# Optimization experiments

Hardware: AMD Instinct MI355X
Metric: run time of the kernel (lower is better)

The kernel has to match this reference:

```python
import jax, jax.numpy as jnp
import numpy as np

ALPHA = 1.0

def setup_inputs() -> dict:
    key = jax.random.key(0)
    k1, k2 = jax.random.split(key)
    x = jax.random.normal(k1, (65536, 512), dtype=jnp.float32)
    clusters = jax.random.normal(k2, (256, 512), dtype=jnp.float32)
    return {"x": x, "clusters": clusters}

def reference(x, clusters):
    # Squared Euclidean distance to each centroid via the GEMM expansion
    x2 = jnp.sum(x * x, axis=1, keepdims=True)            # (B, 1)
    c2 = jnp.sum(clusters * clusters, axis=1)             # (K,)
    cross = x @ clusters.T                                # (B, K) GEMM
    d2 = jnp.maximum(x2 + c2 - 2.0 * cross, 0.0)          # (B, K)
    # Student-t kernel (DEC soft assignment)
    q = 1.0 / (1.0 + d2 / ALPHA)
    q = q ** ((ALPHA + 1.0) / 2.0)
    q = q / jnp.sum(q, axis=1, keepdims=True)             # row-normalize
    return q
```

## Files before the change

kernel.cpp:

```cpp
#include <hip/hip_runtime.h>
#include <hip/hip_bf16.h>


typedef __attribute__((ext_vector_type(8))) short short8v;
typedef __attribute__((ext_vector_type(4))) float f32x4;

#define DDIM 512
#define KCL  256
#define BM   64
#define NT   256
#define NTILES 16
#define BTILE  8192

__device__ __forceinline__ short f2bf(float f) {
    __hip_bfloat16 h = __float2bfloat16(f);
    return __builtin_bit_cast(short, h);
}

__device__ __forceinline__ void glds16(const void* g, void* l) {
    __builtin_amdgcn_global_load_lds(
        (const __attribute__((address_space(1))) unsigned int*)g,
        (__attribute__((address_space(3))) unsigned int*)l, 16, 0, 0);
}

__global__ void prep(const float* __restrict__ cl, short* __restrict__ wsB,
                     float* __restrict__ wsC2) {
    const int t = threadIdx.x;
    if (blockIdx.x < 64) {
        const int u = blockIdx.x * 256 + t;
        const int img = u >> 10, gi = u & 1023;
        const int g = gi >> 6, lq = (gi >> 4) & 3, l15 = gi & 15;
        const float* src = cl + (size_t)(g * 16 + l15) * DDIM + img * 32 + lq * 8;
        float4 a = *(const float4*)src;
        float4 b = *(const float4*)(src + 4);
        short8v s;
        s[0]=f2bf(a.x); s[1]=f2bf(a.y); s[2]=f2bf(a.z); s[3]=f2bf(a.w);
        s[4]=f2bf(b.x); s[5]=f2bf(b.y); s[6]=f2bf(b.z); s[7]=f2bf(b.w);
        *(short8v*)&wsB[(size_t)u * 8] = s;
    } else {
        const int cidx = (blockIdx.x - 64) * 16 + (t >> 4);
        const int j = t & 15;
        const float* src = cl + (size_t)cidx * DDIM + j * 32;
        float s = 0.f;
#pragma unroll
        for (int i = 0; i < 8; ++i) {
            float4 v = ((const float4*)src)[i];
            s += v.x*v.x + v.y*v.y + v.z*v.z + v.w*v.w;
        }
        s += __shfl_xor(s, 1); s += __shfl_xor(s, 2);
        s += __shfl_xor(s, 4); s += __shfl_xor(s, 8);
        if (j == 0) wsC2[cidx] = s;
    }
}

#define SFENCE() __builtin_amdgcn_sched_barrier(0)
#define BARV0()  asm volatile("s_waitcnt vmcnt(0) lgkmcnt(0)\ns_barrier" ::: "memory")

__global__ __launch_bounds__(NT, 3)
void dec_main(const float* __restrict__ x, const short* __restrict__ wsB,
              const float* __restrict__ wsC2, float* __restrict__ out) {
    __shared__ __align__(16) short lBd[2][BTILE];
    __shared__ __align__(16) float lAf[2][2048];
    __shared__ float s_x2[BM];
    __shared__ float s_rs[4][BM];

    const int t = threadIdx.x, lane = t & 63, w = t >> 6;
    const int cg = w;
    const int l15 = lane & 15, lq = lane >> 4;
    const int row0 = blockIdx.x * BM;

    const int rA = ((t >> 7) << 4) + (t & 15);
    const int cA = (((t >> 4) & 3) << 3) + (((t >> 6) & 1) << 2);
    const float* ga0 = x + (size_t)(row0 + rA) * DDIM + cA;
    const float* ga1 = x + (size_t)(row0 + rA + 32) * DDIM + cA;

    f32x4 acc[4][4];
#pragma unroll
    for (int m = 0; m < 4; ++m)
#pragma unroll
        for (int n = 0; n < 4; ++n) acc[m][n] = (f32x4){0.f,0.f,0.f,0.f};
    float x2p[4] = {0.f, 0.f, 0.f, 0.f};

#define GLDSA(TT, P)                                                 \
    {  glds16(ga0 + (TT) * 32, &lAf[P][t * 4]);                      \
       glds16(ga1 + (TT) * 32, &lAf[P][t * 4 + 1024]); }

#define GLDSB(TT, P)                                                 \
    {  const short* s_ = wsB + (size_t)(TT) * BTILE;                 \
       short* d_ = &lBd[P][0];                                       \
       glds16(s_ + t * 8,        d_ + t * 8);                        \
       glds16(s_ + 2048 + t * 8, d_ + 2048 + t * 8);                 \
       glds16(s_ + 4096 + t * 8, d_ + 4096 + t * 8);                 \
       glds16(s_ + 6144 + t * 8, d_ + 6144 + t * 8); }

#define MSTEP(P)                                                                 \
    {  short8v b0 = *(const short8v*)&lBd[P][(cg*4+0)*512 + lane*8];             \
       short8v b1 = *(const short8v*)&lBd[P][(cg*4+1)*512 + lane*8];             \
       short8v b2 = *(const short8v*)&lBd[P][(cg*4+2)*512 + lane*8];             \
       short8v b3 = *(const short8v*)&lBd[P][(cg*4+3)*512 + lane*8];             \
       _Pragma("unroll")                                                         \
       for (int m = 0; m < 4; ++m) {                                             \
           float4 alo = *(const float4*)&lAf[P][m*512 + lane*4];                 \
           float4 ahi = *(const float4*)&lAf[P][m*512 + 256 + lane*4];           \
           short8v af;                                                           \
           af[0]=f2bf(alo.x); af[1]=f2bf(alo.y); af[2]=f2bf(alo.z); af[3]=f2bf(alo.w); \
           af[4]=f2bf(ahi.x); af[5]=f2bf(ahi.y); af[6]=f2bf(ahi.z); af[7]=f2bf(ahi.w); \
           if (w == 0)                                                           \
               x2p[m] += alo.x*alo.x + alo.y*alo.y + alo.z*alo.z + alo.w*alo.w   \
                       + ahi.x*ahi.x + ahi.y*ahi.y + ahi.z*ahi.z + ahi.w*ahi.w;  \
           acc[m][0] = __builtin_amdgcn_mfma_f32_16x16x32_bf16(af, b0, acc[m][0], 0,0,0); \
           acc[m][1] = __builtin_amdgcn_mfma_f32_16x16x32_bf16(af, b1, acc[m][1], 0,0,0); \
           acc[m][2] = __builtin_amdgcn_mfma_f32_16x16x32_bf16(af, b2, acc[m][2], 0,0,0); \
           acc[m][3] = __builtin_amdgcn_mfma_f32_16x16x32_bf16(af, b3, acc[m][3], 0,0,0); \
       } }

#define ITER(J)                                                                  \
    {  if ((J) + 1 < NTILES) { GLDSA((J)+1, ((J)+1)&1); GLDSB((J)+1, ((J)+1)&1); } \
       SFENCE();                                                                 \
       MSTEP((J)&1);                                                             \
       if ((J) + 1 < NTILES) { BARV0(); }                                        \
       SFENCE(); }

    GLDSA(0, 0); GLDSB(0, 0);
    BARV0();
    SFENCE();

    ITER( 0) ITER( 1) ITER( 2) ITER( 3)
    ITER( 4) ITER( 5) ITER( 6) ITER( 7)
    ITER( 8) ITER( 9) ITER(10) ITER(11)
    ITER(12) ITER(13) ITER(14) ITER(15)

#pragma unroll
    for (int m = 0; m < 4; ++m) {
        float v = x2p[m];
        v += __shfl_xor(v, 16); v += __shfl_xor(v, 32);
        if (w == 0 && lq == 0) s_x2[m*16 + l15] = v;
    }
    __syncthreads();

    float c2a[4];
#pragma unroll
    for (int n = 0; n < 4; ++n) c2a[n] = wsC2[cg*64 + n*16 + l15];

#pragma unroll
    for (int m = 0; m < 4; ++m)
#pragma unroll
        for (int n = 0; n < 4; ++n)
#pragma unroll
            for (int r = 0; r < 4; ++r) {
                const int rw = m*16 + lq*4 + r;
                float d2 = fmaxf(s_x2[rw] + c2a[n] - 2.0f * acc[m][n][r], 0.0f);
                acc[m][n][r] = 1.0f / (1.0f + d2);
            }

#pragma unroll
    for (int m = 0; m < 4; ++m)
#pragma unroll
        for (int r = 0; r < 4; ++r) {
            float p = acc[m][0][r] + acc[m][1][r] + acc[m][2][r] + acc[m][3][r];
            p += __shfl_xor(p, 1); p += __shfl_xor(p, 2);
            p += __shfl_xor(p, 4); p += __shfl_xor(p, 8);
            if (l15 == 0) s_rs[cg][m*16 + lq*4 + r] = p;
        }
    __syncthreads();

#pragma unroll
    for (int m = 0; m < 4; ++m)
#pragma unroll
        for (int r = 0; r < 4; ++r) {
            const int rw = m*16 + lq*4 + r;
            const float rinv = 1.0f / (s_rs[0][rw] + s_rs[1][rw] + s_rs[2][rw] + s_rs[3][rw]);
            float* o = out + (size_t)(row0 + rw) * KCL + cg*64 + l15;
#pragma unroll
            for (int n = 0; n < 4; ++n)
                o[n * 16] = acc[m][n][r] * rinv;
        }
}

extern "C" void kernel_launch(void* const* d_in, const int* in_sizes, int n_in,
                              void* d_out, int out_size, void* d_ws, size_t ws_size,
                              hipStream_t stream) {
    const float* x  = (const float*)d_in[0];
    const float* cl = (const float*)d_in[1];
    float* out = (float*)d_out;
    short* wsB  = (short*)d_ws;
    float* wsC2 = (float*)((char*)d_ws + (size_t)NTILES * BTILE * sizeof(short));

    prep<<<80, 256, 0, stream>>>(cl, wsB, wsC2);
    const int B = in_sizes[0] / DDIM;
    dec_main<<<B / BM, NT, 0, stream>>>(x, wsB, wsC2, out);
}
```

Before: 60.26 us.

## Double block tile to 128 rows and prefetch A two stages ahead

Doubles the rows per block to 128 with 512 threads (8 waves, split into 2 row groups x 4 column groups), so each staged centroid tile is reused across twice as many rows and B-loading per thread halves. The x tile now uses a triple-buffered LDS ring loaded two iterations ahead, and barriers wait with vmcnt(2) so the next A load can stay in flight across the barrier. Scratch arrays for row norms and row sums reuse the A buffer, with an extra barrier added before reuse. LDS per block grows to about 80KB and the grid halves, which may reduce occupancy and the number of blocks available per CU.

```diff
diff --git a/kernel.cpp b/kernel.cpp
--- a/kernel.cpp
+++ b/kernel.cpp
@@ -7,8 +7,8 @@
 
 #define DDIM 512
 #define KCL  256
-#define BM   64
-#define NT   256
+#define BM   128
+#define NT   512
 #define NTILES 16
 #define BTILE  8192
 
@@ -54,25 +54,26 @@
 }
 
 #define SFENCE() __builtin_amdgcn_sched_barrier(0)
+#define BARV2()  asm volatile("s_waitcnt vmcnt(2) lgkmcnt(0)\ns_barrier" ::: "memory")
 #define BARV0()  asm volatile("s_waitcnt vmcnt(0) lgkmcnt(0)\ns_barrier" ::: "memory")
 
-__global__ __launch_bounds__(NT, 3)
+__global__ __launch_bounds__(NT, 4)
 void dec_main(const float* __restrict__ x, const short* __restrict__ wsB,
               const float* __restrict__ wsC2, float* __restrict__ out) {
+    __shared__ __align__(16) float lAf[3][4096];
     __shared__ __align__(16) short lBd[2][BTILE];
-    __shared__ __align__(16) float lAf[2][2048];
-    __shared__ float s_x2[BM];
-    __shared__ float s_rs[4][BM];
+    float* const s_x2 = &lAf[0][0];
+    float* const s_rs = &lAf[0][0] + BM;
 
     const int t = threadIdx.x, lane = t & 63, w = t >> 6;
-    const int cg = w;
+    const int rg = w >> 2, cg = w & 3;
     const int l15 = lane & 15, lq = lane >> 4;
     const int row0 = blockIdx.x * BM;
 
     const int rA = ((t >> 7) << 4) + (t & 15);
     const int cA = (((t >> 4) & 3) << 3) + (((t >> 6) & 1) << 2);
     const float* ga0 = x + (size_t)(row0 + rA) * DDIM + cA;
-    const float* ga1 = x + (size_t)(row0 + rA + 32) * DDIM + cA;
+    const float* ga1 = x + (size_t)(row0 + rA + 64) * DDIM + cA;
 
     f32x4 acc[4][4];
 #pragma unroll
@@ -83,29 +84,26 @@
 
 #define GLDSA(TT, P)                                                 \
     {  glds16(ga0 + (TT) * 32, &lAf[P][t * 4]);                      \
-       glds16(ga1 + (TT) * 32, &lAf[P][t * 4 + 1024]); }
+       glds16(ga1 + (TT) * 32, &lAf[P][t * 4 + 2048]); }
 
 #define GLDSB(TT, P)                                                 \
     {  const short* s_ = wsB + (size_t)(TT) * BTILE;                 \
-       short* d_ = &lBd[P][0];                                       \
-       glds16(s_ + t * 8,        d_ + t * 8);                        \
-       glds16(s_ + 2048 + t * 8, d_ + 2048 + t * 8);                 \
-       glds16(s_ + 4096 + t * 8, d_ + 4096 + t * 8);                 \
-       glds16(s_ + 6144 + t * 8, d_ + 6144 + t * 8); }
-
-#define MSTEP(P)                                                                 \
-    {  short8v b0 = *(const short8v*)&lBd[P][(cg*4+0)*512 + lane*8];             \
-       short8v b1 = *(const short8v*)&lBd[P][(cg*4+1)*512 + lane*8];             \
-       short8v b2 = *(const short8v*)&lBd[P][(cg*4+2)*512 + lane*8];             \
-       short8v b3 = *(const short8v*)&lBd[P][(cg*4+3)*512 + lane*8];             \
+       glds16(s_ + t * 8,        &lBd[P][t * 8]);                    \
+       glds16(s_ + 4096 + t * 8, &lBd[P][4096 + t * 8]); }
+
+#define MSTEP(AP, BP)                                                            \
+    {  short8v b0 = *(const short8v*)&lBd[BP][(cg*4+0)*512 + lane*8];            \
+       short8v b1 = *(const short8v*)&lBd[BP][(cg*4+1)*512 + lane*8];            \
+       short8v b2 = *(const short8v*)&lBd[BP][(cg*4+2)*512 + lane*8];            \
+       short8v b3 = *(const short8v*)&lBd[BP][(cg*4+3)*512 + lane*8];            \
        _Pragma("unroll")                                                         \
        for (int m = 0; m < 4; ++m) {                                             \
-           float4 alo = *(const float4*)&lAf[P][m*512 + lane*4];                 \
-           float4 ahi = *(const float4*)&lAf[P][m*512 + 256 + lane*4];           \
+           float4 alo = *(const float4*)&lAf[AP][(rg*4+m)*512 + lane*4];         \
+           float4 ahi = *(const float4*)&lAf[AP][(rg*4+m)*512 + 256 + lane*4];   \
            short8v af;                                                           \
            af[0]=f2bf(alo.x); af[1]=f2bf(alo.y); af[2]=f2bf(alo.z); af[3]=f2bf(alo.w); \
            af[4]=f2bf(ahi.x); af[5]=f2bf(ahi.y); af[6]=f2bf(ahi.z); af[7]=f2bf(ahi.w); \
-           if (w == 0)                                                           \
+           if (cg == 0)                                                          \
                x2p[m] += alo.x*alo.x + alo.y*alo.y + alo.z*alo.z + alo.w*alo.w   \
                        + ahi.x*ahi.x + ahi.y*ahi.y + ahi.z*ahi.z + ahi.w*ahi.w;  \
            acc[m][0] = __builtin_amdgcn_mfma_f32_16x16x32_bf16(af, b0, acc[m][0], 0,0,0); \
@@ -114,27 +112,46 @@
            acc[m][3] = __builtin_amdgcn_mfma_f32_16x16x32_bf16(af, b3, acc[m][3], 0,0,0); \
        } }
 
-#define ITER(J)                                                                  \
-    {  if ((J) + 1 < NTILES) { GLDSA((J)+1, ((J)+1)&1); GLDSB((J)+1, ((J)+1)&1); } \
+#define ITER(J, AC, AN, BC, BN)                                                  \
+    {  if ((J) + 1 < NTILES) { GLDSB((J)+1, BN); }                               \
+       if ((J) + 2 < NTILES) { GLDSA((J)+2, AN); }                               \
        SFENCE();                                                                 \
-       MSTEP((J)&1);                                                             \
-       if ((J) + 1 < NTILES) { BARV0(); }                                        \
+       MSTEP(AC, BC);                                                            \
+       SFENCE();                                                                 \
+       if ((J) + 2 < NTILES) { BARV2(); }                                        \
+       else if ((J) + 1 < NTILES) { BARV0(); }                                   \
        SFENCE(); }
 
-    GLDSA(0, 0); GLDSB(0, 0);
-    BARV0();
+    GLDSA(0, 0);
+    GLDSB(0, 0);
+    GLDSA(1, 1);
     SFENCE();
-
-    ITER( 0) ITER( 1) ITER( 2) ITER( 3)
-    ITER( 4) ITER( 5) ITER( 6) ITER( 7)
-    ITER( 8) ITER( 9) ITER(10) ITER(11)
-    ITER(12) ITER(13) ITER(14) ITER(15)
-
+    BARV2();
+    SFENCE();
+
+    ITER( 0, 0, 2, 0, 1)
+    ITER( 1, 1, 0, 1, 0)
+    ITER( 2, 2, 1, 0, 1)
+    ITER( 3, 0, 2, 1, 0)
+    ITER( 4, 1, 0, 0, 1)
+    ITER( 5, 2, 1, 1, 0)
+    ITER( 6, 0, 2, 0, 1)
+    ITER( 7, 1, 0, 1, 0)
+    ITER( 8, 2, 1, 0, 1)
+    ITER( 9, 0, 2, 1, 0)
+    ITER(10, 1, 0, 0, 1)
+    ITER(11, 2, 1, 1, 0)
+    ITER(12, 0, 2, 0, 1)
+    ITER(13, 1, 0, 1, 0)
+    ITER(14, 2, 1, 0, 1)
+    ITER(15, 0, 0, 1, 1)
+
+    __syncthreads();
 #pragma unroll
     for (int m = 0; m < 4; ++m) {
         float v = x2p[m];
         v += __shfl_xor(v, 16); v += __shfl_xor(v, 32);
-        if (w == 0 && lq == 0) s_x2[m*16 + l15] = v;
+        if (cg == 0 && lq == 0) s_x2[rg*64 + m*16 + l15] = v;
     }
     __syncthreads();
 
@@ -148,7 +165,7 @@
         for (int n = 0; n < 4; ++n)
 #pragma unroll
             for (int r = 0; r < 4; ++r) {
-                const int rw = m*16 + lq*4 + r;
+                const int rw = rg*64 + m*16 + lq*4 + r;
                 float d2 = fmaxf(s_x2[rw] + c2a[n] - 2.0f * acc[m][n][r], 0.0f);
                 acc[m][n][r] = 1.0f / (1.0f + d2);
             }
@@ -160,7 +177,7 @@
             float p = acc[m][0][r] + acc[m][1][r] + acc[m][2][r] + acc[m][3][r];
             p += __shfl_xor(p, 1); p += __shfl_xor(p, 2);
             p += __shfl_xor(p, 4); p += __shfl_xor(p, 8);
-            if (l15 == 0) s_rs[cg][m*16 + lq*4 + r] = p;
+            if (l15 == 0) s_rs[cg*BM + rg*64 + m*16 + lq*4 + r] = p;
         }
     __syncthreads();
 
@@ -168,8 +185,9 @@
     for (int m = 0; m < 4; ++m)
 #pragma unroll
         for (int r = 0; r < 4; ++r) {
-            const int rw = m*16 + lq*4 + r;
-            const float rinv = 1.0f / (s_rs[0][rw] + s_rs[1][rw] + s_rs[2][rw] + s_rs[3][rw]);
+            const int rw = rg*64 + m*16 + lq*4 + r;
+            const float rinv = 1.0f / (s_rs[rw] + s_rs[BM + rw]
+                                     + s_rs[2*BM + rw] + s_rs[3*BM + rw]);
             float* o = out + (size_t)(row0 + rw) * KCL + cg*64 + l15;
 #pragma unroll
             for (int n = 0; n < 4; ++n)
```

After: 50.19 us. 1.2x faster.

## Load centroid operands into registers and deepen A-tile LDS pipeline to 4 stages

Applied to the files above, without the earlier changes.

The bf16 centroid tiles are now read straight from global memory into double-buffered registers per wave, instead of being staged through shared memory. The x tiles use a 4-slot LDS ring prefetched three tiles ahead. Barriers now wait only on LDS counters, with a partial vmcnt wait in the prologue. Launch bounds rise to 4 blocks per CU, helped by the smaller LDS footprint. The aim is to hide global latency and cut LDS traffic. The risk is that the in-loop barriers no longer wait for other waves' global-to-LDS copies, which relies on timing slack, and register pressure goes up.

```diff
diff --git a/kernel.cpp b/kernel.cpp
--- a/kernel.cpp
+++ b/kernel.cpp
@@ -53,26 +53,27 @@
     }
 }
 
-#define SFENCE() __builtin_amdgcn_sched_barrier(0)
-#define BARV0()  asm volatile("s_waitcnt vmcnt(0) lgkmcnt(0)\ns_barrier" ::: "memory")
-
-__global__ __launch_bounds__(NT, 3)
+#define SFENCE()  __builtin_amdgcn_sched_barrier(0)
+#define BARLGKM() asm volatile("s_waitcnt lgkmcnt(0)\ns_barrier" ::: "memory")
+#define BARP()    asm volatile("s_waitcnt vmcnt(8) lgkmcnt(0)\ns_barrier" ::: "memory")
+
+__global__ __launch_bounds__(NT, 4)
 void dec_main(const float* __restrict__ x, const short* __restrict__ wsB,
               const float* __restrict__ wsC2, float* __restrict__ out) {
-    __shared__ __align__(16) short lBd[2][BTILE];
-    __shared__ __align__(16) float lAf[2][2048];
+    __shared__ __align__(16) float lAf[4][2048];
     __shared__ float s_x2[BM];
     __shared__ float s_rs[4][BM];
 
-    const int t = threadIdx.x, lane = t & 63, w = t >> 6;
-    const int cg = w;
+    const int t = threadIdx.x, lane = t & 63, cg = t >> 6;
     const int l15 = lane & 15, lq = lane >> 4;
     const int row0 = blockIdx.x * BM;
 
     const int rA = ((t >> 7) << 4) + (t & 15);
     const int cA = (((t >> 4) & 3) << 3) + (((t >> 6) & 1) << 2);
     const float* ga0 = x + (size_t)(row0 + rA) * DDIM + cA;
-    const float* ga1 = x + (size_t)(row0 + rA + 32) * DDIM + cA;
+    const float* ga1 = ga0 + (size_t)32 * DDIM;
+
+    const short* bb = wsB + (size_t)cg * 2048 + (size_t)lane * 8;
 
     f32x4 acc[4][4];
 #pragma unroll
@@ -80,61 +81,78 @@
 #pragma unroll
         for (int n = 0; n < 4; ++n) acc[m][n] = (f32x4){0.f,0.f,0.f,0.f};
     float x2p[4] = {0.f, 0.f, 0.f, 0.f};
+    short8v Ba[4], Bb[4];
 
 #define GLDSA(TT, P)                                                 \
     {  glds16(ga0 + (TT) * 32, &lAf[P][t * 4]);                      \
        glds16(ga1 + (TT) * 32, &lAf[P][t * 4 + 1024]); }
 
-#define GLDSB(TT, P)                                                 \
-    {  const short* s_ = wsB + (size_t)(TT) * BTILE;                 \
-       short* d_ = &lBd[P][0];                                       \
-       glds16(s_ + t * 8,        d_ + t * 8);                        \
-       glds16(s_ + 2048 + t * 8, d_ + 2048 + t * 8);                 \
-       glds16(s_ + 4096 + t * 8, d_ + 4096 + t * 8);                 \
-       glds16(s_ + 6144 + t * 8, d_ + 6144 + t * 8); }
-
-#define MSTEP(P)                                                                 \
-    {  short8v b0 = *(const short8v*)&lBd[P][(cg*4+0)*512 + lane*8];             \
-       short8v b1 = *(const short8v*)&lBd[P][(cg*4+1)*512 + lane*8];             \
-       short8v b2 = *(const short8v*)&lBd[P][(cg*4+2)*512 + lane*8];             \
-       short8v b3 = *(const short8v*)&lBd[P][(cg*4+3)*512 + lane*8];             \
-       _Pragma("unroll")                                                         \
+#define LOADB(TT, S)                                                 \
+    {  const short* bt = bb + (size_t)(TT) * BTILE;                  \
+       S[0] = *(const short8v*)(bt);                                 \
+       S[1] = *(const short8v*)(bt + 512);                           \
+       S[2] = *(const short8v*)(bt + 1024);                          \
+       S[3] = *(const short8v*)(bt + 1536); }
+
+#define MSTEP(P, S)                                                              \
+    {  _Pragma("unroll")                                                         \
        for (int m = 0; m < 4; ++m) {                                             \
            float4 alo = *(const float4*)&lAf[P][m*512 + lane*4];                 \
            float4 ahi = *(const float4*)&lAf[P][m*512 + 256 + lane*4];           \
            short8v af;                                                           \
            af[0]=f2bf(alo.x); af[1]=f2bf(alo.y); af[2]=f2bf(alo.z); af[3]=f2bf(alo.w); \
            af[4]=f2bf(ahi.x); af[5]=f2bf(ahi.y); af[6]=f2bf(ahi.z); af[7]=f2bf(ahi.w); \
-           if (w == 0)                                                           \
+           if (cg == 0)                                                          \
                x2p[m] += alo.x*alo.x + alo.y*alo.y + alo.z*alo.z + alo.w*alo.w   \
                        + ahi.x*ahi.x + ahi.y*ahi.y + ahi.z*ahi.z + ahi.w*ahi.w;  \
-           acc[m][0] = __builtin_amdgcn_mfma_f32_16x16x32_bf16(af, b0, acc[m][0], 0,0,0); \
-           acc[m][1] = __builtin_amdgcn_mfma_f32_16x16x32_bf16(af, b1, acc[m][1], 0,0,0); \
-           acc[m][2] = __builtin_amdgcn_mfma_f32_16x16x32_bf16(af, b2, acc[m][2], 0,0,0); \
-           acc[m][3] = __builtin_amdgcn_mfma_f32_16x16x32_bf16(af, b3, acc[m][3], 0,0,0); \
+           acc[m][0] = __builtin_amdgcn_mfma_f32_16x16x32_bf16(af, S[0], acc[m][0], 0,0,0); \
+           acc[m][1] = __builtin_amdgcn_mfma_f32_16x16x32_bf16(af, S[1], acc[m][1], 0,0,0); \
+           acc[m][2] = __builtin_amdgcn_mfma_f32_16x16x32_bf16(af, S[2], acc[m][2], 0,0,0); \
+           acc[m][3] = __builtin_amdgcn_mfma_f32_16x16x32_bf16(af, S[3], acc[m][3], 0,0,0); \
        } }
 
-#define ITER(J)                                                                  \
-    {  if ((J) + 1 < NTILES) { GLDSA((J)+1, ((J)+1)&1); GLDSB((J)+1, ((J)+1)&1); } \
+#define ITER(J, BCUR, BNXT)                                                      \
+    {  if ((J) + 1 < NTILES) { LOADB((J)+1, BNXT); }                             \
        SFENCE();                                                                 \
-       MSTEP((J)&1);                                                             \
-       if ((J) + 1 < NTILES) { BARV0(); }                                        \
+       if ((J) + 3 < NTILES) { GLDSA((J)+3, ((J)+3)&3); }                        \
+       SFENCE();                                                                 \
+       MSTEP((J)&3, BCUR);                                                       \
+       SFENCE();                                                                 \
+       if ((J) + 1 < NTILES) { BARLGKM(); }                                      \
        SFENCE(); }
 
-    GLDSA(0, 0); GLDSB(0, 0);
-    BARV0();
-    SFENCE();
-
-    ITER( 0) ITER( 1) ITER( 2) ITER( 3)
-    ITER( 4) ITER( 5) ITER( 6) ITER( 7)
-    ITER( 8) ITER( 9) ITER(10) ITER(11)
-    ITER(12) ITER(13) ITER(14) ITER(15)
+    GLDSA(0, 0);
+    GLDSA(1, 1);
+    SFENCE();
+    LOADB(0, Ba);
+    SFENCE();
+    GLDSA(2, 2);
+    SFENCE();
+    BARP();
+    SFENCE();
+
+    ITER( 0, Ba, Bb)
+    ITER( 1, Bb, Ba)
+    ITER( 2, Ba, Bb)
+    ITER( 3, Bb, Ba)
+    ITER( 4, Ba, Bb)
+    ITER( 5, Bb, Ba)
+    ITER( 6, Ba, Bb)
+    ITER( 7, Bb, Ba)
+    ITER( 8, Ba, Bb)
+    ITER( 9, Bb, Ba)
+    ITER(10, Ba, Bb)
+    ITER(11, Bb, Ba)
+    ITER(12, Ba, Bb)
+    ITER(13, Bb, Ba)
+    ITER(14, Ba, Bb)
+    ITER(15, Bb, Ba)
 
 #pragma unroll
     for (int m = 0; m < 4; ++m) {
         float v = x2p[m];
         v += __shfl_xor(v, 16); v += __shfl_xor(v, 32);
-        if (w == 0 && lq == 0) s_x2[m*16 + l15] = v;
+        if (cg == 0 && lq == 0) s_x2[m*16 + l15] = v;
     }
     __syncthreads();
 
```

After: 51.15 us. 1.18x faster.
